# Kernel tuning notes

Measured on AMD Instinct MI355X. Metric: run time of the kernel, lower is better.

The kernel has to match this reference:

```python
import jax, jax.numpy as jnp
import numpy as np

B, N, D, H, DH, DEPTH, VOCAB, MULT = 4, 1024, 768, 12, 64, 6, 32000, 4
INNER = H * DH
FF = D * MULT
EPS = 1e-6


def setup_inputs() -> dict:
    key = jax.random.key(0)
    ks = jax.random.split(key, 9)
    s = lambda fan: 1.0 / np.sqrt(fan)
    return {
        "tokens": jax.random.randint(ks[0], (B, N), 0, VOCAB, dtype=jnp.int32),
        "mask": jnp.ones((B, N), dtype=bool),
        "embed": jax.random.normal(ks[1], (VOCAB, D), jnp.float32),
        "wq": jax.random.normal(ks[2], (DEPTH, INNER, D), jnp.float32) * s(D),
        "wk": jax.random.normal(ks[3], (DEPTH, INNER, D), jnp.float32) * s(D),
        "wv": jax.random.normal(ks[4], (DEPTH, INNER, D), jnp.float32) * s(D),
        "wo": jax.random.normal(ks[5], (DEPTH, D, INNER), jnp.float32) * s(INNER),
        "wi": jax.random.normal(ks[6], (DEPTH, FF, D), jnp.float32) * s(D),
        "wof": jax.random.normal(ks[7], (DEPTH, D, FF), jnp.float32) * s(FF),
        "ln_w": jnp.ones((D,), jnp.float32),
    }


def _t5_layernorm(x, w):
    var = jnp.mean(jnp.square(x.astype(jnp.float32)), axis=-1, keepdims=True)
    return w * (x * jax.lax.rsqrt(var + EPS))


def reference(tokens, mask, embed, wq, wk, wv, wo, wi, wof, ln_w):
    x = embed[tokens]  # [B, N, D]
    scale = DH ** -0.5
    neg = -jnp.finfo(x.dtype).max
    m = mask[:, None, :, None]  # masks query rows, as in the torch code
    for l in range(DEPTH):
        # attention (no pre-LN: WrapperBlock never calls its layer_norm)
        q = (x @ wq[l].T).reshape(B, N, H, DH).transpose(0, 2, 1, 3) * scale
        k = (x @ wk[l].T).reshape(B, N, H, DH).transpose(0, 2, 1, 3)
        v = (x @ wv[l].T).reshape(B, N, H, DH).transpose(0, 2, 1, 3)
        sim = jnp.einsum('bhid,bhjd->bhij', q, k)
        sim = jnp.where(m, sim, neg)
        attn = jax.nn.softmax(sim, axis=-1)
        o = jnp.einsum('bhij,bhjd->bhid', attn, v)
        o = o.transpose(0, 2, 1, 3).reshape(B, N, INNER) @ wo[l].T
        x = x + o
        # feed-forward
        y = jax.nn.relu(x @ wi[l].T) @ wof[l].T
        x = x + y
    return _t5_layernorm(x, ln_w)
```

## Files before the change

### kernel.cpp

```cpp
#include <hip/hip_runtime.h>
#include <cstdint>

#define NB 4
#define NSEQ 1024
#define DMODEL 768
#define NHEAD 12
#define DHEAD 64
#define NDEPTH 6
#define DFF 3072
#define MROWS (NB * NSEQ)

#define WQ_OFF 0L
#define WK_OFF 589824L
#define WV_OFF 1179648L
#define WO_OFF 1769472L
#define WI_OFF 2359296L
#define WOF_OFF 4718592L
#define WTOT 7077888L

typedef __attribute__((ext_vector_type(8))) short short8;
typedef __attribute__((ext_vector_type(4))) float floatx4;

static __device__ __forceinline__ float b2f(unsigned short u) {
  union { unsigned int i; float f; } v; v.i = ((unsigned int)u) << 16; return v.f;
}
static __device__ __forceinline__ unsigned short f2b(float f) {
  union { float f; unsigned int i; } v; v.f = f;
  unsigned int x = v.i;
  return (unsigned short)((x + 0x7fffu + ((x >> 16) & 1u)) >> 16);
}
static __device__ __forceinline__ void fsplit(float f, unsigned short& h, unsigned short& l) {
  h = f2b(f);
  l = f2b(f - b2f(h));
}

__global__ __launch_bounds__(256) void wsplit_kernel(
    const float* __restrict__ wq, const float* __restrict__ wk,
    const float* __restrict__ wv, const float* __restrict__ wo,
    const float* __restrict__ wi, const float* __restrict__ wof,
    unsigned short* __restrict__ dhi, unsigned short* __restrict__ dlo)
{
  long i = ((long)blockIdx.x * 256 + threadIdx.x) * 4;
  if (i >= WTOT) return;
  const float* src; long off;
  if (i < WK_OFF)       { src = wq;  off = i - WQ_OFF; }
  else if (i < WV_OFF)  { src = wk;  off = i - WK_OFF; }
  else if (i < WO_OFF)  { src = wv;  off = i - WV_OFF; }
  else if (i < WI_OFF)  { src = wo;  off = i - WO_OFF; }
  else if (i < WOF_OFF) { src = wi;  off = i - WI_OFF; }
  else                  { src = wof; off = i - WOF_OFF; }
  float4 f = *(const float4*)(src + off);
  ushort4 h, l;
  fsplit(f.x, h.x, l.x); fsplit(f.y, h.y, l.y);
  fsplit(f.z, h.z, l.z); fsplit(f.w, h.w, l.w);
  *(ushort4*)(dhi + i) = h;
  *(ushort4*)(dlo + i) = l;
}

__global__ void embed_kernel(const int* __restrict__ tok,
                             const float* __restrict__ emb,
                             unsigned short* __restrict__ xhi,
                             unsigned short* __restrict__ xlo) {
  const int row = blockIdx.x;
  const int t = tok[row];
  const float* src = emb + (long)t * DMODEL;
  for (int d = threadIdx.x; d < DMODEL; d += 256) {
    unsigned short h, l;
    fsplit(src[d], h, l);
    xhi[(long)row * DMODEL + d] = h;
    xlo[(long)row * DMODEL + d] = l;
  }
}

template<int RELU, int RESID>
__global__ __launch_bounds__(256) void gemm_bt(
    const unsigned short* __restrict__ Ahi, const unsigned short* __restrict__ Alo,
    const unsigned short* __restrict__ Whi, const unsigned short* __restrict__ Wlo,
    unsigned short* __restrict__ Chi, unsigned short* __restrict__ Clo,
    const unsigned short* __restrict__ Rhi, const unsigned short* __restrict__ Rlo,
    int M, int N, int K, float alpha)
{
  __shared__ unsigned short sAh[64][40];
  __shared__ unsigned short sAl[64][40];
  __shared__ unsigned short sBh[64][40];
  __shared__ unsigned short sBl[64][40];

  const int tid = threadIdx.x;
  const int bn = blockIdx.x, bm = blockIdx.y;
  const int srow = tid >> 2;
  const int skc  = (tid & 3) << 3;
  const int wave = tid >> 6;
  const int lane = tid & 63;
  const int wm = wave >> 1, wn = wave & 1;
  const int l16 = lane & 15, q4 = lane >> 4;

  floatx4 acc[2][2];
  #pragma unroll
  for (int i = 0; i < 2; ++i)
    #pragma unroll
    for (int j = 0; j < 2; ++j) {
      floatx4 z = {0.f, 0.f, 0.f, 0.f};
      acc[i][j] = z;
    }

  const long arow = (long)(bm * 64 + srow) * K;
  const long brow = (long)(bn * 64 + srow) * K;

  for (int k0 = 0; k0 < K; k0 += 32) {
    *(short8*)&sAh[srow][skc] = *(const short8*)(Ahi + arow + k0 + skc);
    *(short8*)&sAl[srow][skc] = *(const short8*)(Alo + arow + k0 + skc);
    *(short8*)&sBh[srow][skc] = *(const short8*)(Whi + brow + k0 + skc);
    *(short8*)&sBl[srow][skc] = *(const short8*)(Wlo + brow + k0 + skc);
    __syncthreads();

    short8 a0h = *(const short8*)&sAh[wm * 32 +      l16][q4 * 8];
    short8 a1h = *(const short8*)&sAh[wm * 32 + 16 + l16][q4 * 8];
    short8 a0l = *(const short8*)&sAl[wm * 32 +      l16][q4 * 8];
    short8 a1l = *(const short8*)&sAl[wm * 32 + 16 + l16][q4 * 8];
    short8 b0h = *(const short8*)&sBh[wn * 32 +      l16][q4 * 8];
    short8 b1h = *(const short8*)&sBh[wn * 32 + 16 + l16][q4 * 8];
    short8 b0l = *(const short8*)&sBl[wn * 32 +      l16][q4 * 8];
    short8 b1l = *(const short8*)&sBl[wn * 32 + 16 + l16][q4 * 8];

    acc[0][0] = __builtin_amdgcn_mfma_f32_16x16x32_bf16(a0h, b0h, acc[0][0], 0, 0, 0);
    acc[0][1] = __builtin_amdgcn_mfma_f32_16x16x32_bf16(a0h, b1h, acc[0][1], 0, 0, 0);
    acc[1][0] = __builtin_amdgcn_mfma_f32_16x16x32_bf16(a1h, b0h, acc[1][0], 0, 0, 0);
    acc[1][1] = __builtin_amdgcn_mfma_f32_16x16x32_bf16(a1h, b1h, acc[1][1], 0, 0, 0);
    acc[0][0] = __builtin_amdgcn_mfma_f32_16x16x32_bf16(a0l, b0h, acc[0][0], 0, 0, 0);
    acc[0][1] = __builtin_amdgcn_mfma_f32_16x16x32_bf16(a0l, b1h, acc[0][1], 0, 0, 0);
    acc[1][0] = __builtin_amdgcn_mfma_f32_16x16x32_bf16(a1l, b0h, acc[1][0], 0, 0, 0);
    acc[1][1] = __builtin_amdgcn_mfma_f32_16x16x32_bf16(a1l, b1h, acc[1][1], 0, 0, 0);
    acc[0][0] = __builtin_amdgcn_mfma_f32_16x16x32_bf16(a0h, b0l, acc[0][0], 0, 0, 0);
    acc[0][1] = __builtin_amdgcn_mfma_f32_16x16x32_bf16(a0h, b1l, acc[0][1], 0, 0, 0);
    acc[1][0] = __builtin_amdgcn_mfma_f32_16x16x32_bf16(a1h, b0l, acc[1][0], 0, 0, 0);
    acc[1][1] = __builtin_amdgcn_mfma_f32_16x16x32_bf16(a1h, b1l, acc[1][1], 0, 0, 0);
    __syncthreads();
  }

  #pragma unroll
  for (int mt = 0; mt < 2; ++mt) {
    #pragma unroll
    for (int nt = 0; nt < 2; ++nt) {
      const int r0 = bm * 64 + wm * 32 + mt * 16 + q4 * 4;
      const int c  = bn * 64 + wn * 32 + nt * 16 + l16;
      #pragma unroll
      for (int r = 0; r < 4; ++r) {
        float vv = acc[mt][nt][r] * alpha;
        const long idx = (long)(r0 + r) * N + c;
        if (RESID) vv += b2f(Rhi[idx]) + b2f(Rlo[idx]);
        if (RELU)  vv = fmaxf(vv, 0.f);
        unsigned short h, l;
        fsplit(vv, h, l);
        Chi[idx] = h; Clo[idx] = l;
      }
    }
  }
}

__global__ __launch_bounds__(256) void attn_kernel(
    const unsigned short* __restrict__ qhi, const unsigned short* __restrict__ qlo,
    const unsigned short* __restrict__ khi, const unsigned short* __restrict__ klo,
    const unsigned short* __restrict__ vhi, const unsigned short* __restrict__ vlo,
    unsigned short* __restrict__ ohi, unsigned short* __restrict__ olo)
{
  __shared__ unsigned short ks_h[64][72];
  __shared__ unsigned short ks_l[64][72];
  __shared__ unsigned short vt_h[64][72];
  __shared__ unsigned short vt_l[64][72];
  __shared__ unsigned short ps_h[64][72];
  __shared__ unsigned short ps_l[64][72];

  const int tid = threadIdx.x;
  const int iq = blockIdx.x, h = blockIdx.y, b = blockIdx.z;
  const int wave = tid >> 6, lane = tid & 63;
  const int l16 = lane & 15, g4 = lane >> 4;
  const long base = ((long)b * NSEQ) * DMODEL + h * DHEAD;
  const int q0 = iq * 64;

  short8 qh[2], ql[2];
  {
    const long qr = base + (long)(q0 + wave * 16 + l16) * DMODEL + g4 * 8;
    qh[0] = *(const short8*)(qhi + qr);
    qh[1] = *(const short8*)(qhi + qr + 32);
    ql[0] = *(const short8*)(qlo + qr);
    ql[1] = *(const short8*)(qlo + qr + 32);
  }

  floatx4 oacc[4];
  #pragma unroll
  for (int nt = 0; nt < 4; ++nt) { floatx4 z = {0.f,0.f,0.f,0.f}; oacc[nt] = z; }
  float mrow[4] = {-INFINITY, -INFINITY, -INFINITY, -INFINITY};
  float lrow[4] = {0.f, 0.f, 0.f, 0.f};

  const int skey = tid >> 3;
  const int sd0  = (tid & 7) * 8;

  for (int jc = 0; jc < NSEQ / 64; ++jc) {
    const int j0 = jc * 64;
    if (jc) __syncthreads();

    #pragma unroll
    for (int half = 0; half < 2; ++half) {
      const int key = skey + half * 32;
      const long off = base + (long)(j0 + key) * DMODEL + sd0;
      short8 kh8 = *(const short8*)(khi + off);
      short8 kl8 = *(const short8*)(klo + off);
      short8 vh8 = *(const short8*)(vhi + off);
      short8 vl8 = *(const short8*)(vlo + off);
      *(short8*)&ks_h[key][sd0] = kh8;
      *(short8*)&ks_l[key][sd0] = kl8;
      #pragma unroll
      for (int u = 0; u < 8; ++u) {
        const int dh = sd0 + u;
        const int cc = key ^ ((dh >> 3) << 3);
        vt_h[dh][cc] = (unsigned short)vh8[u];
        vt_l[dh][cc] = (unsigned short)vl8[u];
      }
    }
    __syncthreads();

    floatx4 sacc[4];
    #pragma unroll
    for (int nt = 0; nt < 4; ++nt) { floatx4 z = {0.f,0.f,0.f,0.f}; sacc[nt] = z; }
    #pragma unroll
    for (int nt = 0; nt < 4; ++nt) {
      #pragma unroll
      for (int ks = 0; ks < 2; ++ks) {
        short8 kh8 = *(const short8*)&ks_h[nt * 16 + l16][ks * 32 + g4 * 8];
        short8 kl8 = *(const short8*)&ks_l[nt * 16 + l16][ks * 32 + g4 * 8];
        sacc[nt] = __builtin_amdgcn_mfma_f32_16x16x32_bf16(qh[ks], kh8, sacc[nt], 0, 0, 0);
        sacc[nt] = __builtin_amdgcn_mfma_f32_16x16x32_bf16(ql[ks], kh8, sacc[nt], 0, 0, 0);
        sacc[nt] = __builtin_amdgcn_mfma_f32_16x16x32_bf16(qh[ks], kl8, sacc[nt], 0, 0, 0);
      }
    }

    float mx[4], al[4];
    #pragma unroll
    for (int r = 0; r < 4; ++r) {
      float m0 = fmaxf(fmaxf(sacc[0][r], sacc[1][r]), fmaxf(sacc[2][r], sacc[3][r]));
      m0 = fmaxf(m0, __shfl_xor(m0, 1));
      m0 = fmaxf(m0, __shfl_xor(m0, 2));
      m0 = fmaxf(m0, __shfl_xor(m0, 4));
      m0 = fmaxf(m0, __shfl_xor(m0, 8));
      const float mn = fmaxf(mrow[r], m0);
      al[r] = __expf(mrow[r] - mn);
      mrow[r] = mn;
      mx[r] = mn;
    }
    #pragma unroll
    for (int r = 0; r < 4; ++r) {
      const int qrow = wave * 16 + g4 * 4 + r;
      float rs = 0.f;
      #pragma unroll
      for (int nt = 0; nt < 4; ++nt) {
        const float p = __expf(sacc[nt][r] - mx[r]);
        rs += p;
        unsigned short ph, pl;
        fsplit(p, ph, pl);
        ps_h[qrow][nt * 16 + l16] = ph;
        ps_l[qrow][nt * 16 + l16] = pl;
      }
      rs += __shfl_xor(rs, 1);
      rs += __shfl_xor(rs, 2);
      rs += __shfl_xor(rs, 4);
      rs += __shfl_xor(rs, 8);
      lrow[r] = lrow[r] * al[r] + rs;
      oacc[0][r] *= al[r]; oacc[1][r] *= al[r];
      oacc[2][r] *= al[r]; oacc[3][r] *= al[r];
    }
    __syncthreads();

    #pragma unroll
    for (int ks = 0; ks < 2; ++ks) {
      short8 ph8 = *(const short8*)&ps_h[wave * 16 + l16][ks * 32 + g4 * 8];
      short8 pl8 = *(const short8*)&ps_l[wave * 16 + l16][ks * 32 + g4 * 8];
      #pragma unroll
      for (int nt = 0; nt < 4; ++nt) {
        const int dh = nt * 16 + l16;
        const int cb = (ks * 32 + g4 * 8) ^ ((dh >> 3) << 3);
        short8 vh8 = *(const short8*)&vt_h[dh][cb];
        short8 vl8 = *(const short8*)&vt_l[dh][cb];
        oacc[nt] = __builtin_amdgcn_mfma_f32_16x16x32_bf16(ph8, vh8, oacc[nt], 0, 0, 0);
        oacc[nt] = __builtin_amdgcn_mfma_f32_16x16x32_bf16(pl8, vh8, oacc[nt], 0, 0, 0);
        oacc[nt] = __builtin_amdgcn_mfma_f32_16x16x32_bf16(ph8, vl8, oacc[nt], 0, 0, 0);
      }
    }
  }

  const long orbase = base + (long)(q0 + wave * 16 + g4 * 4) * DMODEL;
  #pragma unroll
  for (int r = 0; r < 4; ++r) {
    const float inv = 1.f / lrow[r];
    #pragma unroll
    for (int nt = 0; nt < 4; ++nt) {
      unsigned short hh, ll;
      fsplit(oacc[nt][r] * inv, hh, ll);
      const long idx = orbase + (long)r * DMODEL + nt * 16 + l16;
      ohi[idx] = hh; olo[idx] = ll;
    }
  }
}

__global__ __launch_bounds__(256) void ln_kernel(const unsigned short* __restrict__ xhi,
                                                 const unsigned short* __restrict__ xlo,
                                                 const float* __restrict__ w,
                                                 float* __restrict__ out)
{
  __shared__ float red[256];
  const int row = blockIdx.x;
  const long rb = (long)row * DMODEL;
  float ss = 0.f;
  for (int d = threadIdx.x; d < DMODEL; d += 256) {
    float v = b2f(xhi[rb + d]) + b2f(xlo[rb + d]);
    ss += v * v;
  }
  red[threadIdx.x] = ss;
  __syncthreads();
  for (int s = 128; s > 0; s >>= 1) {
    if (threadIdx.x < s) red[threadIdx.x] += red[threadIdx.x + s];
    __syncthreads();
  }
  const float rs = rsqrtf(red[0] * (1.f / DMODEL) + 1e-6f);
  for (int d = threadIdx.x; d < DMODEL; d += 256) {
    float v = b2f(xhi[rb + d]) + b2f(xlo[rb + d]);
    out[rb + d] = w[d] * v * rs;
  }
}

extern "C" void kernel_launch(void* const* d_in, const int* in_sizes, int n_in,
                              void* d_out, int out_size, void* d_ws, size_t ws_size,
                              hipStream_t stream)
{
  const int* tokens   = (const int*)d_in[0];
  const float* emb    = (const float*)d_in[2];
  const float* wq     = (const float*)d_in[3];
  const float* wk     = (const float*)d_in[4];
  const float* wv     = (const float*)d_in[5];
  const float* wo     = (const float*)d_in[6];
  const float* wi     = (const float*)d_in[7];
  const float* wof    = (const float*)d_in[8];
  const float* lnw    = (const float*)d_in[9];

  const size_t AS = (size_t)MROWS * DMODEL;
  char* p = (char*)d_ws;
  unsigned short* xhi = (unsigned short*)p;  p += AS * 2;
  unsigned short* xlo = (unsigned short*)p;  p += AS * 2;
  unsigned short* act = (unsigned short*)p;  p += AS * 2 * 8;
  unsigned short* whi = (unsigned short*)p;  p += (size_t)WTOT * 2;
  unsigned short* wlo = (unsigned short*)p;  p += (size_t)WTOT * 2;

  unsigned short* qhi = act + AS * 0; unsigned short* qlo = act + AS * 1;
  unsigned short* khi = act + AS * 2; unsigned short* klo = act + AS * 3;
  unsigned short* vhi = act + AS * 4; unsigned short* vlo = act + AS * 5;
  unsigned short* ohi = act + AS * 6; unsigned short* olo = act + AS * 7;
  unsigned short* fhi = act + AS * 0; unsigned short* flo = act + AS * 4;

  embed_kernel<<<MROWS, 256, 0, stream>>>(tokens, emb, xhi, xlo);

  const dim3 g768(DMODEL / 64, MROWS / 64);
  const dim3 gff(DFF / 64, MROWS / 64);
  const dim3 gattn(NSEQ / 64, NHEAD, NB);
  const int splitblocks = (int)(WTOT / 1024);

  for (int l = 0; l < NDEPTH; ++l) {
    wsplit_kernel<<<splitblocks, 256, 0, stream>>>(
        wq  + (size_t)l * DMODEL * DMODEL,
        wk  + (size_t)l * DMODEL * DMODEL,
        wv  + (size_t)l * DMODEL * DMODEL,
        wo  + (size_t)l * DMODEL * DMODEL,
        wi  + (size_t)l * DFF * DMODEL,
        wof + (size_t)l * DMODEL * DFF,
        whi, wlo);

    gemm_bt<0, 0><<<g768, 256, 0, stream>>>(xhi, xlo, whi + WQ_OFF, wlo + WQ_OFF,
                                            qhi, qlo, nullptr, nullptr,
                                            MROWS, DMODEL, DMODEL, 0.125f);
    gemm_bt<0, 0><<<g768, 256, 0, stream>>>(xhi, xlo, whi + WK_OFF, wlo + WK_OFF,
                                            khi, klo, nullptr, nullptr,
                                            MROWS, DMODEL, DMODEL, 1.f);
    gemm_bt<0, 0><<<g768, 256, 0, stream>>>(xhi, xlo, whi + WV_OFF, wlo + WV_OFF,
                                            vhi, vlo, nullptr, nullptr,
                                            MROWS, DMODEL, DMODEL, 1.f);
    attn_kernel<<<gattn, 256, 0, stream>>>(qhi, qlo, khi, klo, vhi, vlo, ohi, olo);
    gemm_bt<0, 1><<<g768, 256, 0, stream>>>(ohi, olo, whi + WO_OFF, wlo + WO_OFF,
                                            xhi, xlo, xhi, xlo,
                                            MROWS, DMODEL, DMODEL, 1.f);
    gemm_bt<1, 0><<<gff, 256, 0, stream>>>(xhi, xlo, whi + WI_OFF, wlo + WI_OFF,
                                           fhi, flo, nullptr, nullptr,
                                           MROWS, DFF, DMODEL, 1.f);
    gemm_bt<0, 1><<<g768, 256, 0, stream>>>(fhi, flo, whi + WOF_OFF, wlo + WOF_OFF,
                                            xhi, xlo, xhi, xlo,
                                            MROWS, DMODEL, DFF, 1.f);
  }

  ln_kernel<<<MROWS, 256, 0, stream>>>(xhi, xlo, lnw, (float*)d_out);
}
```

Before: 2.779 ms.

## Fuse QKV projections and enlarge GEMM tiles with direct global-to-LDS loads

Replaces the 64x64 GEMM with a templated kernel that uses 128-wide N tiles (and 128 or 64 row tiles) and per-wave 4x4 or 4x2 MFMA sub-tiles. Global-to-LDS copies now use global_load_lds, which skips the register round trip. The three Q/K/V projections are fused into one GEMM writing an interleaved [M,2304] buffer, relying on the contiguous WQ/WK/WV weight layout, and Q scaling is applied per column. This is meant to raise data reuse per LDS load and cut launches, at the cost of more registers and LDS, unpadded LDS rows that may cause bank conflicts, and fewer blocks for the 768-wide GEMMs.

Result: faster. 2.510 ms (-9.7%).

```diff
diff --git a/kernel.cpp b/kernel.cpp
--- a/kernel.cpp
+++ b/kernel.cpp
@@ -9,6 +9,7 @@
 #define NDEPTH 6
 #define DFF 3072
 #define MROWS (NB * NSEQ)
+#define QKVLD 2304
 
 #define WQ_OFF 0L
 #define WK_OFF 589824L
@@ -32,6 +33,12 @@
 static __device__ __forceinline__ void fsplit(float f, unsigned short& h, unsigned short& l) {
   h = f2b(f);
   l = f2b(f - b2f(h));
+}
+
+static __device__ __forceinline__ void gload16(const unsigned short* g, unsigned short* l) {
+  __builtin_amdgcn_global_load_lds(
+      (const __attribute__((address_space(1))) void*)g,
+      (__attribute__((address_space(3))) void*)l, 16, 0, 0);
 }
 
 __global__ __launch_bounds__(256) void wsplit_kernel(
@@ -72,80 +79,97 @@
   }
 }
 
-template<int RELU, int RESID>
-__global__ __launch_bounds__(256) void gemm_bt(
+template<int BM, int WGM, int WGN, int MT, int NT, int RELU, int RESID, int QSCALE>
+__global__ __launch_bounds__(256) void gemm128(
     const unsigned short* __restrict__ Ahi, const unsigned short* __restrict__ Alo,
     const unsigned short* __restrict__ Whi, const unsigned short* __restrict__ Wlo,
     unsigned short* __restrict__ Chi, unsigned short* __restrict__ Clo,
     const unsigned short* __restrict__ Rhi, const unsigned short* __restrict__ Rlo,
-    int M, int N, int K, float alpha)
+    int N, int K, float alpha)
 {
-  __shared__ unsigned short sAh[64][40];
-  __shared__ unsigned short sAl[64][40];
-  __shared__ unsigned short sBh[64][40];
-  __shared__ unsigned short sBl[64][40];
+  __shared__ unsigned short sAh[BM * 32];
+  __shared__ unsigned short sAl[BM * 32];
+  __shared__ unsigned short sBh[128 * 32];
+  __shared__ unsigned short sBl[128 * 32];
 
   const int tid = threadIdx.x;
   const int bn = blockIdx.x, bm = blockIdx.y;
+  const int wave = tid >> 6, lane = tid & 63;
+  const int wm = wave / WGN, wn = wave % WGN;
+  const int l16 = lane & 15, q4 = lane >> 4;
+
   const int srow = tid >> 2;
-  const int skc  = (tid & 3) << 3;
-  const int wave = tid >> 6;
-  const int lane = tid & 63;
-  const int wm = wave >> 1, wn = wave & 1;
-  const int l16 = lane & 15, q4 = lane >> 4;
-
-  floatx4 acc[2][2];
+  const int scol = (tid & 3) << 3;
+  const int soff = tid * 8;
+
+  floatx4 acc[MT][NT];
   #pragma unroll
-  for (int i = 0; i < 2; ++i)
-    #pragma unroll
-    for (int j = 0; j < 2; ++j) {
+  for (int i = 0; i < MT; ++i)
+    #pragma unroll
+    for (int j = 0; j < NT; ++j) {
       floatx4 z = {0.f, 0.f, 0.f, 0.f};
       acc[i][j] = z;
     }
 
-  const long arow = (long)(bm * 64 + srow) * K;
-  const long brow = (long)(bn * 64 + srow) * K;
+  const long aB = ((long)bm * BM + srow) * K + scol;
+  const long bB = ((long)bn * 128 + srow) * K + scol;
 
   for (int k0 = 0; k0 < K; k0 += 32) {
-    *(short8*)&sAh[srow][skc] = *(const short8*)(Ahi + arow + k0 + skc);
-    *(short8*)&sAl[srow][skc] = *(const short8*)(Alo + arow + k0 + skc);
-    *(short8*)&sBh[srow][skc] = *(const short8*)(Whi + brow + k0 + skc);
-    *(short8*)&sBl[srow][skc] = *(const short8*)(Wlo + brow + k0 + skc);
+    #pragma unroll
+    for (int c = 0; c < BM / 64; ++c) {
+      gload16(Ahi + aB + (long)c * 64 * K + k0, sAh + c * 2048 + soff);
+      gload16(Alo + aB + (long)c * 64 * K + k0, sAl + c * 2048 + soff);
+    }
+    #pragma unroll
+    for (int c = 0; c < 2; ++c) {
+      gload16(Whi + bB + (long)c * 64 * K + k0, sBh + c * 2048 + soff);
+      gload16(Wlo + bB + (long)c * 64 * K + k0, sBl + c * 2048 + soff);
+    }
     __syncthreads();
 
-    short8 a0h = *(const short8*)&sAh[wm * 32 +      l16][q4 * 8];
-    short8 a1h = *(const short8*)&sAh[wm * 32 + 16 + l16][q4 * 8];
-    short8 a0l = *(const short8*)&sAl[wm * 32 +      l16][q4 * 8];
-    short8 a1l = *(const short8*)&sAl[wm * 32 + 16 + l16][q4 * 8];
-    short8 b0h = *(const short8*)&sBh[wn * 32 +      l16][q4 * 8];
-    short8 b1h = *(const short8*)&sBh[wn * 32 + 16 + l16][q4 * 8];
-    short8 b0l = *(const short8*)&sBl[wn * 32 +      l16][q4 * 8];
-    short8 b1l = *(const short8*)&sBl[wn * 32 + 16 + l16][q4 * 8];
-
-    acc[0][0] = __builtin_amdgcn_mfma_f32_16x16x32_bf16(a0h, b0h, acc[0][0], 0, 0, 0);
-    acc[0][1] = __builtin_amdgcn_mfma_f32_16x16x32_bf16(a0h, b1h, acc[0][1], 0, 0, 0);
-    acc[1][0] = __builtin_amdgcn_mfma_f32_16x16x32_bf16(a1h, b0h, acc[1][0], 0, 0, 0);
-    acc[1][1] = __builtin_amdgcn_mfma_f32_16x16x32_bf16(a1h, b1h, acc[1][1], 0, 0, 0);
-    acc[0][0] = __builtin_amdgcn_mfma_f32_16x16x32_bf16(a0l, b0h, acc[0][0], 0, 0, 0);
-    acc[0][1] = __builtin_amdgcn_mfma_f32_16x16x32_bf16(a0l, b1h, acc[0][1], 0, 0, 0);
-    acc[1][0] = __builtin_amdgcn_mfma_f32_16x16x32_bf16(a1l, b0h, acc[1][0], 0, 0, 0);
-    acc[1][1] = __builtin_amdgcn_mfma_f32_16x16x32_bf16(a1l, b1h, acc[1][1], 0, 0, 0);
-    acc[0][0] = __builtin_amdgcn_mfma_f32_16x16x32_bf16(a0h, b0l, acc[0][0], 0, 0, 0);
-    acc[0][1] = __builtin_amdgcn_mfma_f32_16x16x32_bf16(a0h, b1l, acc[0][1], 0, 0, 0);
-    acc[1][0] = __builtin_amdgcn_mfma_f32_16x16x32_bf16(a1h, b0l, acc[1][0], 0, 0, 0);
-    acc[1][1] = __builtin_amdgcn_mfma_f32_16x16x32_bf16(a1h, b1l, acc[1][1], 0, 0, 0);
+    short8 ah[MT], al[MT], bh[NT], bl[NT];
+    #pragma unroll
+    for (int mt = 0; mt < MT; ++mt) {
+      const int row = wm * (MT * 16) + mt * 16 + l16;
+      ah[mt] = *(const short8*)&sAh[row * 32 + q4 * 8];
+      al[mt] = *(const short8*)&sAl[row * 32 + q4 * 8];
+    }
+    #pragma unroll
+    for (int nt = 0; nt < NT; ++nt) {
+      const int row = wn * (NT * 16) + nt * 16 + l16;
+      bh[nt] = *(const short8*)&sBh[row * 32 + q4 * 8];
+      bl[nt] = *(const short8*)&sBl[row * 32 + q4 * 8];
+    }
+
+    #pragma unroll
+    for (int mt = 0; mt < MT; ++mt)
+      #pragma unroll
+      for (int nt = 0; nt < NT; ++nt)
+        acc[mt][nt] = __builtin_amdgcn_mfma_f32_16x16x32_bf16(ah[mt], bh[nt], acc[mt][nt], 0, 0, 0);
+    #pragma unroll
+    for (int mt = 0; mt < MT; ++mt)
+      #pragma unroll
+      for (int nt = 0; nt < NT; ++nt)
+        acc[mt][nt] = __builtin_amdgcn_mfma_f32_16x16x32_bf16(al[mt], bh[nt], acc[mt][nt], 0, 0, 0);
+    #pragma unroll
+    for (int mt = 0; mt < MT; ++mt)
+      #pragma unroll
+      for (int nt = 0; nt < NT; ++nt)
+        acc[mt][nt] = __builtin_amdgcn_mfma_f32_16x16x32_bf16(ah[mt], bl[nt], acc[mt][nt], 0, 0, 0);
     __syncthreads();
   }
 
   #pragma unroll
-  for (int mt = 0; mt < 2; ++mt) {
-    #pragma unroll
-    for (int nt = 0; nt < 2; ++nt) {
-      const int r0 = bm * 64 + wm * 32 + mt * 16 + q4 * 4;
-      const int c  = bn * 64 + wn * 32 + nt * 16 + l16;
+  for (int mt = 0; mt < MT; ++mt) {
+    const int r0 = bm * BM + wm * (MT * 16) + mt * 16 + q4 * 4;
+    #pragma unroll
+    for (int nt = 0; nt < NT; ++nt) {
+      const int c = bn * 128 + wn * (NT * 16) + nt * 16 + l16;
+      float sc = alpha;
+      if (QSCALE) sc = (c < DMODEL) ? alpha : 1.f;
       #pragma unroll
       for (int r = 0; r < 4; ++r) {
-        float vv = acc[mt][nt][r] * alpha;
+        float vv = acc[mt][nt][r] * sc;
         const long idx = (long)(r0 + r) * N + c;
         if (RESID) vv += b2f(Rhi[idx]) + b2f(Rlo[idx]);
         if (RELU)  vv = fmaxf(vv, 0.f);
@@ -158,9 +182,7 @@
 }
 
 __global__ __launch_bounds__(256) void attn_kernel(
-    const unsigned short* __restrict__ qhi, const unsigned short* __restrict__ qlo,
-    const unsigned short* __restrict__ khi, const unsigned short* __restrict__ klo,
-    const unsigned short* __restrict__ vhi, const unsigned short* __restrict__ vlo,
+    const unsigned short* __restrict__ qkvhi, const unsigned short* __restrict__ qkvlo,
     unsigned short* __restrict__ ohi, unsigned short* __restrict__ olo)
 {
   __shared__ unsigned short ks_h[64][72];
@@ -174,16 +196,19 @@
   const int iq = blockIdx.x, h = blockIdx.y, b = blockIdx.z;
   const int wave = tid >> 6, lane = tid & 63;
   const int l16 = lane & 15, g4 = lane >> 4;
-  const long base = ((long)b * NSEQ) * DMODEL + h * DHEAD;
+  const long qb = ((long)b * NSEQ) * QKVLD + h * DHEAD;
+  const long kb = qb + DMODEL;
+  const long vb = qb + 2 * DMODEL;
+  const long ob = ((long)b * NSEQ) * DMODEL + h * DHEAD;
   const int q0 = iq * 64;
 
   short8 qh[2], ql[2];
   {
-    const long qr = base + (long)(q0 + wave * 16 + l16) * DMODEL + g4 * 8;
-    qh[0] = *(const short8*)(qhi + qr);
-    qh[1] = *(const short8*)(qhi + qr + 32);
-    ql[0] = *(const short8*)(qlo + qr);
-    ql[1] = *(const short8*)(qlo + qr + 32);
+    const long qr = qb + (long)(q0 + wave * 16 + l16) * QKVLD + g4 * 8;
+    qh[0] = *(const short8*)(qkvhi + qr);
+    qh[1] = *(const short8*)(qkvhi + qr + 32);
+    ql[0] = *(const short8*)(qkvlo + qr);
+    ql[1] = *(const short8*)(qkvlo + qr + 32);
   }
 
   floatx4 oacc[4];
@@ -202,11 +227,12 @@
     #pragma unroll
     for (int half = 0; half < 2; ++half) {
       const int key = skey + half * 32;
-      const long off = base + (long)(j0 + key) * DMODEL + sd0;
-      short8 kh8 = *(const short8*)(khi + off);
-      short8 kl8 = *(const short8*)(klo + off);
-      short8 vh8 = *(const short8*)(vhi + off);
-      short8 vl8 = *(const short8*)(vlo + off);
+      const long offk = kb + (long)(j0 + key) * QKVLD + sd0;
+      const long offv = vb + (long)(j0 + key) * QKVLD + sd0;
+      short8 kh8 = *(const short8*)(qkvhi + offk);
+      short8 kl8 = *(const short8*)(qkvlo + offk);
+      short8 vh8 = *(const short8*)(qkvhi + offv);
+      short8 vl8 = *(const short8*)(qkvlo + offv);
       *(short8*)&ks_h[key][sd0] = kh8;
       *(short8*)&ks_l[key][sd0] = kl8;
       #pragma unroll
@@ -287,7 +313,7 @@
     }
   }
 
-  const long orbase = base + (long)(q0 + wave * 16 + g4 * 4) * DMODEL;
+  const long orbase = ob + (long)(q0 + wave * 16 + g4 * 4) * DMODEL;
   #pragma unroll
   for (int r = 0; r < 4; ++r) {
     const float inv = 1.f / lrow[r];
@@ -349,16 +375,18 @@
   unsigned short* whi = (unsigned short*)p;  p += (size_t)WTOT * 2;
   unsigned short* wlo = (unsigned short*)p;  p += (size_t)WTOT * 2;
 
-  unsigned short* qhi = act + AS * 0; unsigned short* qlo = act + AS * 1;
-  unsigned short* khi = act + AS * 2; unsigned short* klo = act + AS * 3;
-  unsigned short* vhi = act + AS * 4; unsigned short* vlo = act + AS * 5;
-  unsigned short* ohi = act + AS * 6; unsigned short* olo = act + AS * 7;
-  unsigned short* fhi = act + AS * 0; unsigned short* flo = act + AS * 4;
+  unsigned short* qkvhi = act + AS * 0;
+  unsigned short* qkvlo = act + AS * 3;
+  unsigned short* ohi   = act + AS * 6;
+  unsigned short* olo   = act + AS * 7;
+  unsigned short* fhi   = act + AS * 0;
+  unsigned short* flo   = act + AS * 4;
 
   embed_kernel<<<MROWS, 256, 0, stream>>>(tokens, emb, xhi, xlo);
 
-  const dim3 g768(DMODEL / 64, MROWS / 64);
-  const dim3 gff(DFF / 64, MROWS / 64);
+  const dim3 gqkv(QKVLD / 128, MROWS / 128);
+  const dim3 gwo(DMODEL / 128, MROWS / 64);
+  const dim3 gwi(DFF / 128, MROWS / 128);
   const dim3 gattn(NSEQ / 64, NHEAD, NB);
   const int splitblocks = (int)(WTOT / 1024);
 
@@ -372,25 +400,19 @@
         wof + (size_t)l * DMODEL * DFF,
         whi, wlo);
 
-    gemm_bt<0, 0><<<g768, 256, 0, stream>>>(xhi, xlo, whi + WQ_OFF, wlo + WQ_OFF,
-                                            qhi, qlo, nullptr, nullptr,
-                                            MROWS, DMODEL, DMODEL, 0.125f);
-    gemm_bt<0, 0><<<g768, 256, 0, stream>>>(xhi, xlo, whi + WK_OFF, wlo + WK_OFF,
-                                            khi, klo, nullptr, nullptr,
-                                            MROWS, DMODEL, DMODEL, 1.f);
-    gemm_bt<0, 0><<<g768, 256, 0, stream>>>(xhi, xlo, whi + WV_OFF, wlo + WV_OFF,
-                                            vhi, vlo, nullptr, nullptr,
-                                            MROWS, DMODEL, DMODEL, 1.f);
-    attn_kernel<<<gattn, 256, 0, stream>>>(qhi, qlo, khi, klo, vhi, vlo, ohi, olo);
-    gemm_bt<0, 1><<<g768, 256, 0, stream>>>(ohi, olo, whi + WO_OFF, wlo + WO_OFF,
-                                            xhi, xlo, xhi, xlo,
-                                            MROWS, DMODEL, DMODEL, 1.f);
-    gemm_bt<1, 0><<<gff, 256, 0, stream>>>(xhi, xlo, whi + WI_OFF, wlo + WI_OFF,
-                                           fhi, flo, nullptr, nullptr,
-                                           MROWS, DFF, DMODEL, 1.f);
-    gemm_bt<0, 1><<<g768, 256, 0, stream>>>(fhi, flo, whi + WOF_OFF, wlo + WOF_OFF,
-                                            xhi, xlo, xhi, xlo,
-                                            MROWS, DMODEL, DFF, 1.f);
+    gemm128<128,2,2,4,4, 0,0,1><<<gqkv, 256, 0, stream>>>(
+        xhi, xlo, whi + WQ_OFF, wlo + WQ_OFF,
+        qkvhi, qkvlo, nullptr, nullptr, QKVLD, DMODEL, 0.125f);
+    attn_kernel<<<gattn, 256, 0, stream>>>(qkvhi, qkvlo, ohi, olo);
+    gemm128<64,1,4,4,2, 0,1,0><<<gwo, 256, 0, stream>>>(
+        ohi, olo, whi + WO_OFF, wlo + WO_OFF,
+        xhi, xlo, xhi, xlo, DMODEL, DMODEL, 1.f);
+    gemm128<128,2,2,4,4, 1,0,0><<<gwi, 256, 0, stream>>>(
+        xhi, xlo, whi + WI_OFF, wlo + WI_OFF,
+        fhi, flo, nullptr, nullptr, DFF, DMODEL, 1.f);
+    gemm128<64,1,4,4,2, 0,1,0><<<gwo, 256, 0, stream>>>(
+        fhi, flo, whi + WOF_OFF, wlo + WOF_OFF,
+        xhi, xlo, xhi, xlo, DMODEL, DFF, 1.f);
   }
 
   ln_kernel<<<MROWS, 256, 0, stream>>>(xhi, xlo, lnw, (float*)d_out);
```
